# Kernel optimization log

Measured on AMD Instinct MI355X. Metric: run time of the kernel, lower is better.

## Reference

```python
import jax, jax.numpy as jnp
import numpy as np

GAMMA = 1.4
EX = jnp.array([1.0, 0.0], dtype=jnp.float32)
EY = jnp.array([0.0, 1.0], dtype=jnp.float32)


def _mlp(x, Ws, bs):
    h = x
    for W, b in zip(Ws[:-1], bs[:-1]):
        h = jnp.tanh(h @ W + b)
    return h @ Ws[-1] + bs[-1]


def setup_inputs() -> dict:
    key = jax.random.key(0)
    ks = jax.random.split(key, 24)
    N, NB = 32768, 4096
    inp = {}
    dom = jnp.array([1.5, 1.0], dtype=jnp.float32)
    inp['x_train'] = jax.random.uniform(ks[0], (N, 2), dtype=jnp.float32) * dom
    inp['x_inlet'] = jax.random.uniform(ks[1], (NB, 2), dtype=jnp.float32) * dom
    inp['U_inlet'] = jax.random.normal(ks[2], (NB, 4), dtype=jnp.float32)
    inp['x_base'] = jax.random.uniform(ks[3], (NB, 2), dtype=jnp.float32) * dom
    inp['x_top'] = jax.random.uniform(ks[4], (NB, 2), dtype=jnp.float32) * dom
    inp['x_slipNormal'] = jax.random.uniform(ks[5], (NB, 2), dtype=jnp.float32) * dom
    dims = [2, 128, 128, 128, 128, 4]
    for i in range(5):
        fan_in = dims[i]
        inp[f'W{i}'] = jax.random.normal(ks[6 + i], (dims[i], dims[i + 1]), dtype=jnp.float32) / jnp.sqrt(jnp.float32(fan_in))
        inp[f'b{i}'] = jnp.zeros((dims[i + 1],), dtype=jnp.float32)
    d2 = [2, 64, 64, 1]
    for i in range(3):
        inp[f'V{i}'] = jax.random.normal(ks[12 + i], (d2[i], d2[i + 1]), dtype=jnp.float32) / jnp.sqrt(jnp.float32(d2[i]))
        inp[f'c{i}'] = jnp.zeros((d2[i + 1],), dtype=jnp.float32)
    return inp


def reference(x_train, x_inlet, U_inlet, x_base, x_top, x_slipNormal,
              W0, b0, W1, b1, W2, b2, W3, b3, W4, b4,
              V0, c0, V1, c1, V2, c2):
    Ws = [W0, W1, W2, W3, W4]
    bs = [b0, b1, b2, b3, b4]
    Vs = [V0, V1, V2]
    cs = [c0, c1, c2]

    def fields(xy):
        # per-point: returns [U1..U4, f1..f4, g1..g4] (12,)
        rho, p, u, v = _mlp(xy, Ws, bs)
        E = p / (GAMMA - 1.0) + 0.5 * rho * (u * u + v * v)
        return jnp.stack([
            rho, rho * u, rho * v, E,                               # U
            rho * u, rho * u * u + p, rho * u * v, u * (E + p),     # f (x-flux)
            rho * v, rho * u * v, rho * v * v + p, v * (E + p)])    # g (y-flux)

    def dUx(xy):
        return jax.jvp(fields, (xy,), (EX,))[1][:4]

    def dUy(xy):
        return jax.jvp(fields, (xy,), (EY,))[1][:4]

    def point_residual(xy):
        _, dx = jax.jvp(fields, (xy,), (EX,))   # x-derivs of all 12 fields
        _, dy = jax.jvp(fields, (xy,), (EY,))   # y-derivs
        U_xx = jax.jvp(dUx, (xy,), (EX,))[1]    # second derivs (fwd-over-fwd)
        U_yy = jax.jvp(dUy, (xy,), (EY,))[1]
        mu = 0.01 * _mlp(xy, Vs, cs)[0] ** 2
        res = dx[4:8] + dy[8:12] - mu * (U_xx + U_yy)  # (4,)
        return res, mu

    res, mu = jax.vmap(point_residual)(x_train)  # res: (N,4), mu: (N,)
    physics = jnp.sum(jnp.mean(res ** 2, axis=0))  # r1+r2+r3+r4

    out_in = _mlp(x_inlet, Ws, bs)
    inlet = jnp.sum(jnp.mean((out_in - U_inlet) ** 2, axis=0))

    base = jnp.mean(_mlp(x_base, Ws, bs)[:, 3] ** 2)
    top = jnp.mean(_mlp(x_top, Ws, bs)[:, 3] ** 2)

    ang = -jnp.pi / 18.0
    o = _mlp(x_slipNormal, Ws, bs)
    slip = jnp.mean((-o[:, 2] * jnp.sin(ang) + o[:, 3] * jnp.cos(ang)) ** 2)

    total = physics + 10.0 * (inlet + base + top + slip) + 0.1 * jnp.mean(mu ** 2)
    return total
```

## Files before the change

### kernel.cpp

```cpp
#include <hip/hip_runtime.h>

#define NTRAIN 32768
#define NBDY   4096
#define PHYS_BLOCKS (NTRAIN / 64)
#define BDY_BLOCKS  128

#define LDS_BYTES 71680

typedef _Float16 f16x8 __attribute__((ext_vector_type(8)));
typedef __fp16   fp16x2 __attribute__((ext_vector_type(2)));
typedef float    f32x4 __attribute__((ext_vector_type(4)));

union FragU { uint4 q; f16x8 b; _Float16 e[8]; };
union F4  { float4 v; float f[4]; };
union H2  { fp16x2 h; _Float16 e[2]; unsigned int u; };

__device__ __forceinline__ float fast_tanh(float z) {
    float e = __expf(2.0f * z);
    return 1.0f - 2.0f * __builtin_amdgcn_rcpf(e + 1.0f);
}

__device__ __forceinline__ unsigned int pk2(float a, float b) {
    H2 r; r.h = __builtin_amdgcn_cvt_pkrtz(a, b);
    return r.u;
}

__global__ __launch_bounds__(256) void pack_w_kernel(
    const float* __restrict__ W1, const float* __restrict__ W2,
    const float* __restrict__ W3, const float* __restrict__ V1,
    const float* __restrict__ W4,
    unsigned short* __restrict__ wsU, float* __restrict__ out)
{
    int b = blockIdx.x;
    if (b < 24) {
        int mat = b >> 3, rb = b & 7;
        const float* W = (mat == 0) ? W1 : (mat == 1) ? W2 : W3;
        unsigned int* hiU = (unsigned int*)(wsU + mat * 32768);
        unsigned int* loU = hiU + 8192;
        int n   = threadIdx.x & 127;
        int pr0 = threadIdx.x >> 7;
        #pragma unroll
        for (int it = 0; it < 4; it++) {
            int pr = pr0 + 2 * it;
            int k  = rb * 16 + pr * 2;
            float v0 = W[k * 128 + n];
            float v1 = W[(k + 1) * 128 + n];
            H2 hh, ll;
            hh.e[0] = (_Float16)v0;
            hh.e[1] = (_Float16)v1;
            ll.e[0] = (_Float16)(v0 - (float)hh.e[0]);
            ll.e[1] = (_Float16)(v1 - (float)hh.e[1]);
            int base = ((n >> 4) * 4 + (k >> 5)) * 64 + ((k >> 3) & 3) * 16 + (n & 15);
            int uoff = base * 4 + ((k & 7) >> 1);
            hiU[uoff] = hh.u;
            loU[uoff] = ll.u;
        }
    } else if (b == 24) {
        unsigned int* hiU = (unsigned int*)(wsU + 98304);
        int n   = threadIdx.x & 63;
        int pr0 = threadIdx.x >> 6;
        #pragma unroll
        for (int it = 0; it < 8; it++) {
            int pr = pr0 + 4 * it;
            int k  = pr * 2;
            float v0 = V1[k * 64 + n];
            float v1 = V1[(k + 1) * 64 + n];
            H2 hh;
            hh.e[0] = (_Float16)v0;
            hh.e[1] = (_Float16)v1;
            int base = ((n >> 4) * 2 + (k >> 5)) * 64 + ((k >> 3) & 3) * 16 + (n & 15);
            hiU[base * 4 + ((k & 7) >> 1)] = hh.u;
        }
        if (threadIdx.x == 0) out[0] = 0.f;
    } else {
        _Float16* hi = (_Float16*)(wsU + 102400);
        _Float16* lo = hi + 2048;
        int u4 = threadIdx.x;
        int lane = u4 & 63, ks = u4 >> 6;
        int m  = lane & 15;
        int kb = ks * 32 + ((lane >> 4) << 3);
        FragU fh, fl;
        #pragma unroll
        for (int j = 0; j < 8; j++) {
            float v = (m < 4) ? W4[(kb + j) * 4 + m] : 0.f;
            _Float16 h = (_Float16)v;
            fh.e[j] = h;
            fl.e[j] = (_Float16)(v - (float)h);
        }
        *(uint4*)(hi + u4 * 8) = fh.q;
        *(uint4*)(lo + u4 * 8) = fl.q;
    }
}

__global__ __launch_bounds__(512, 4) void fused_kernel(
    const float* __restrict__ xt,
    const float* __restrict__ x_inlet, const float* __restrict__ U_inlet,
    const float* __restrict__ x_base,  const float* __restrict__ x_top,
    const float* __restrict__ x_slip,
    const float* __restrict__ W0, const float* __restrict__ b0,
    const float* __restrict__ W1, const float* __restrict__ b1,
    const float* __restrict__ W2, const float* __restrict__ b2,
    const float* __restrict__ W3, const float* __restrict__ b3,
    const float* __restrict__ W4, const float* __restrict__ b4,
    const float* __restrict__ V0, const float* __restrict__ c0,
    const float* __restrict__ V1, const float* __restrict__ c1,
    const float* __restrict__ V2, const float* __restrict__ c2,
    const unsigned short* __restrict__ wsU,
    float* __restrict__ out)
{
    extern __shared__ char SMC[];
    unsigned short* AhU = (unsigned short*)SMC;
    float* MUPART = (float*)(SMC + 69632);
    float* BIASF  = (float*)(SMC + 70144);

    const int t = threadIdx.x;
    const int wv   = t >> 6;
    const int lane = t & 63;
    const int nn   = lane & 15;
    const int q    = lane >> 4;

    if (blockIdx.x < PHYS_BLOCKS) {
        const int blk = blockIdx.x;

        if (t < 128) {
            BIASF[t]       = b1[t];
            BIASF[128 + t] = b2[t];
            BIASF[256 + t] = b3[t];
        }

        {
            const int g = wv >> 1, h = wv & 1;
            const float2 xyn = *(const float2*)(xt + (blk * 64 + g * 16 + nn) * 2);
            FragU mb[2];
            #pragma unroll
            for (int ks = 0; ks < 2; ks++) {
                int u0 = ks * 32 + q * 8;
                F4 va0, va1, vb0, vb1, cc0, cc1;
                va0.v = *(const float4*)(V0 + u0);
                va1.v = *(const float4*)(V0 + u0 + 4);
                vb0.v = *(const float4*)(V0 + 64 + u0);
                vb1.v = *(const float4*)(V0 + 64 + u0 + 4);
                cc0.v = *(const float4*)(c0 + u0);
                cc1.v = *(const float4*)(c0 + u0 + 4);
                #pragma unroll
                for (int i = 0; i < 4; i++) {
                    mb[ks].e[i]     = (_Float16)fast_tanh(
                        xyn.x * va0.f[i] + xyn.y * vb0.f[i] + cc0.f[i]);
                    mb[ks].e[4 + i] = (_Float16)fast_tanh(
                        xyn.x * va1.f[i] + xyn.y * vb1.f[i] + cc1.f[i]);
                }
            }
            float partial = 0.f;
            #pragma unroll
            for (int i = 0; i < 2; i++) {
                f32x4 macc = {0.f, 0.f, 0.f, 0.f};
                #pragma unroll
                for (int ks = 0; ks < 2; ks++) {
                    FragU vh;
                    vh.q = *(const uint4*)(wsU + 98304 +
                           ((((2 * h + i) * 2 + ks) * 64 + lane) << 3));
                    macc = __builtin_amdgcn_mfma_f32_16x16x32_f16(vh.b, mb[ks].b, macc, 0, 0, 0);
                }
                int u2 = (2 * h + i) * 16 + q * 4;
                F4 cv, w2;
                cv.v = *(const float4*)(c1 + u2);
                w2.v = *(const float4*)(V2 + u2);
                #pragma unroll
                for (int r = 0; r < 4; r++)
                    partial += fast_tanh(macc[r] + cv.f[r]) * w2.f[r];
            }
            partial += __shfl_xor(partial, 16);
            partial += __shfl_xor(partial, 32);
            if (lane < 16) MUPART[wv * 16 + nn] = partial;
        }
        {
            const int pl = t >> 4, c = t & 15;
            #pragma unroll
            for (int h2 = 0; h2 < 2; h2++) {
                const int p = h2 * 32 + pl;
                const float2 xy = *(const float2*)(xt + (blk * 64 + p) * 2);
                const float x = xy.x, y = xy.y;
                float vals[4][8];
                #pragma unroll
                for (int j = 0; j < 8; j++) {
                    int u = c * 8 + j;
                    float w0 = W0[u], w1 = W0[128 + u];
                    float zv = x * w0 + y * w1 + b0[u];
                    float tt = fast_tanh(zv);
                    float s2 = 1.f - tt * tt;
                    float m2 = -2.f * tt * s2;
                    vals[0][j] = tt;
                    vals[1][j] = s2 * w0;
                    vals[2][j] = s2 * w1;
                    vals[3][j] = m2 * (w0 * w0 + w1 * w1);
                }
                const int g = p >> 4, p15 = p & 15;
                #pragma unroll
                for (int s = 0; s < 4; s++) {
                    uint4 d = make_uint4(pk2(vals[s][0], vals[s][1]),
                                         pk2(vals[s][2], vals[s][3]),
                                         pk2(vals[s][4], vals[s][5]),
                                         pk2(vals[s][6], vals[s][7]));
                    *(uint4*)(AhU + ((g * 4 + s) * 16 + p15) * 136 + c * 8) = d;
                }
            }
        }
        __syncthreads();

        #pragma unroll 1
        for (int l = 0; l < 3; l++) {
            const unsigned short* WpL = wsU + l * 32768;
            f32x4 acc[16];
            #pragma unroll
            for (int s = 0; s < 16; s++) {
                acc[s][0] = 0.f; acc[s][1] = 0.f;
                acc[s][2] = 0.f; acc[s][3] = 0.f;
            }
            FragU wh[4];
            #pragma unroll
            for (int ks = 0; ks < 4; ks++)
                wh[ks].q = *(const uint4*)(WpL + (((wv * 4 + ks) * 64 + lane) << 3));
            #pragma unroll
            for (int ks = 0; ks < 4; ks++) {
                #pragma unroll
                for (int s = 0; s < 16; s++) {
                    FragU bh;
                    bh.q = *(const uint4*)(AhU + (s * 16 + nn) * 136 + ks * 32 + q * 8);
                    acc[s] = __builtin_amdgcn_mfma_f32_16x16x32_f16(
                        wh[ks].b, bh.b, acc[s], 0, 0, 0);
                }
            }
            __syncthreads();
            const int ubase = wv * 16 + q * 4;
            F4 bv; bv.v = *(const float4*)&BIASF[l * 128 + ubase];
            #pragma unroll
            for (int g = 0; g < 4; g++) {
                float vals[4][4];
                #pragma unroll
                for (int r = 0; r < 4; r++) {
                    float z  = acc[g * 4 + 0][r] + bv.f[r];
                    float zx = acc[g * 4 + 1][r];
                    float zy = acc[g * 4 + 2][r];
                    float zl = acc[g * 4 + 3][r];
                    float tt = fast_tanh(z);
                    float s2 = 1.f - tt * tt;
                    float m2 = -2.f * tt * s2;
                    vals[0][r] = tt;
                    vals[1][r] = s2 * zx;
                    vals[2][r] = s2 * zy;
                    vals[3][r] = s2 * zl + m2 * (zx * zx + zy * zy);
                }
                #pragma unroll
                for (int s = 0; s < 4; s++) {
                    uint2 d = make_uint2(pk2(vals[s][0], vals[s][1]),
                                         pk2(vals[s][2], vals[s][3]));
                    *(uint2*)(AhU + ((g * 4 + s) * 16 + nn) * 136 + ubase) = d;
                }
            }
            __syncthreads();
        }

        {
            const unsigned short* W4p = wsU + 102400;
            const int rtA = wv, rtB = 8 + wv;
            f32x4 aA = {0.f, 0.f, 0.f, 0.f};
            f32x4 aB = {0.f, 0.f, 0.f, 0.f};
            #pragma unroll
            for (int ks = 0; ks < 4; ks++) {
                FragU wh, wl, bA, bB;
                const unsigned short* base = W4p + ((ks * 64 + lane) << 3);
                wh.q = *(const uint4*)base;
                wl.q = *(const uint4*)(base + 2048);
                bA.q = *(const uint4*)(AhU + (rtA * 16 + nn) * 136 + ks * 32 + q * 8);
                bB.q = *(const uint4*)(AhU + (rtB * 16 + nn) * 136 + ks * 32 + q * 8);
                aA = __builtin_amdgcn_mfma_f32_16x16x32_f16(wh.b, bA.b, aA, 0, 0, 0);
                aA = __builtin_amdgcn_mfma_f32_16x16x32_f16(wl.b, bA.b, aA, 0, 0, 0);
                aB = __builtin_amdgcn_mfma_f32_16x16x32_f16(wh.b, bB.b, aB, 0, 0, 0);
                aB = __builtin_amdgcn_mfma_f32_16x16x32_f16(wl.b, bB.b, aB, 0, 0, 0);
            }
            if (q == 0) {
                float4 oA = make_float4(aA[0], aA[1], aA[2], aA[3]);
                float4 oB = make_float4(aB[0], aB[1], aB[2], aB[3]);
                if ((rtA & 3) == 0) {
                    oA.x += b4[0]; oA.y += b4[1]; oA.z += b4[2]; oA.w += b4[3];
                }
                if ((rtB & 3) == 0) {
                    oB.x += b4[0]; oB.y += b4[1]; oB.z += b4[2]; oB.w += b4[3];
                }
                *(float4*)(SMC + (rtA * 16 + nn) * 272 + 256) = oA;
                *(float4*)(SMC + (rtB * 16 + nn) * 272 + 256) = oB;
            }
        }
        __syncthreads();

        float contrib = 0.f;
        if (t < 64) {
            const int pp = t, g = pp >> 4, p15 = pp & 15;
            F4 V, DX, DY, LAP;
            V.v   = *(const float4*)(SMC + ((g * 4 + 0) * 16 + p15) * 272 + 256);
            DX.v  = *(const float4*)(SMC + ((g * 4 + 1) * 16 + p15) * 272 + 256);
            DY.v  = *(const float4*)(SMC + ((g * 4 + 2) * 16 + p15) * 272 + 256);
            LAP.v = *(const float4*)(SMC + ((g * 4 + 3) * 16 + p15) * 272 + 256);
            float r = V.f[0],  P = V.f[1],  u = V.f[2],  v = V.f[3];
            float rx = DX.f[0], Px = DX.f[1], ux = DX.f[2], vx = DX.f[3];
            float ry = DY.f[0], Py = DY.f[1], uy = DY.f[2], vy = DY.f[3];
            float rl = LAP.f[0], Pl = LAP.f[1], ul = LAP.f[2], vl = LAP.f[3];
            const float GI = 2.5f;

            float s = MUPART[(2 * g) * 16 + p15] + MUPART[(2 * g + 1) * 16 + p15]
                    + c2[0];
            float mu = 0.01f * s * s;

            float q2 = u * u + v * v;
            float E  = P * GI + 0.5f * r * q2;
            float Ex = Px * GI + 0.5f * rx * q2 + r * (u * ux + v * vx);
            float Ey = Py * GI + 0.5f * ry * q2 + r * (u * uy + v * vy);
            float EpP = E + P;

            float f1x = rx * u + r * ux;
            float f2x = rx * u * u + 2.f * r * u * ux + Px;
            float f3x = rx * u * v + r * ux * v + r * u * vx;
            float f4x = ux * EpP + u * (Ex + Px);

            float g1y = ry * v + r * vy;
            float g2y = ry * u * v + r * uy * v + r * u * vy;
            float g3y = ry * v * v + 2.f * r * v * vy + Py;
            float g4y = vy * EpP + v * (Ey + Py);

            float qx  = 2.f * (u * ux + v * vx);
            float qy  = 2.f * (u * uy + v * vy);
            float ql  = 2.f * (ux * ux + uy * uy + vx * vx + vy * vy)
                      + 2.f * (u * ul + v * vl);

            float U1s = rl;
            float U2s = rl * u + 2.f * (rx * ux + ry * uy) + r * ul;
            float U3s = rl * v + 2.f * (rx * vx + ry * vy) + r * vl;
            float U4s = Pl * GI
                      + 0.5f * (rl * q2 + 2.f * (rx * qx + ry * qy) + r * ql);

            float r1 = f1x + g1y - mu * U1s;
            float r2 = f2x + g2y - mu * U2s;
            float r3 = f3x + g3y - mu * U3s;
            float r4 = f4x + g4y - mu * U4s;

            contrib = (r1 * r1 + r2 * r2 + r3 * r3 + r4 * r4 + 0.1f * mu * mu)
                      * (1.0f / (float)NTRAIN);
        }
        if (t < 64) {
            contrib += __shfl_down(contrib, 32);
            contrib += __shfl_down(contrib, 16);
            contrib += __shfl_down(contrib, 8);
            contrib += __shfl_down(contrib, 4);
            contrib += __shfl_down(contrib, 2);
            contrib += __shfl_down(contrib, 1);
            if (t == 0) atomicAdd(out, contrib);
        }
    } else {
        const int bb    = blockIdx.x - PHYS_BLOCKS;
        const int batch = bb >> 5;
        const int lb    = bb & 31;
        const float* xs = (batch == 0) ? x_inlet
                        : (batch == 1) ? x_base
                        : (batch == 2) ? x_top : x_slip;
        const int base_pt = lb * 128;

        {
            int p2 = t & 127, ug = t >> 7;
            float2 xy = *(const float2*)(xs + (base_pt + p2) * 2);
            float x = xy.x, y = xy.y;
            #pragma unroll
            for (int g = 0; g < 8; g++) {
                int u0 = ug * 32 + g * 4;
                F4 wa, wb, bbv;
                wa.v  = *(const float4*)(W0 + u0);
                wb.v  = *(const float4*)(W0 + 128 + u0);
                bbv.v = *(const float4*)(b0 + u0);
                float t0 = fast_tanh(x * wa.f[0] + y * wb.f[0] + bbv.f[0]);
                float t1 = fast_tanh(x * wa.f[1] + y * wb.f[1] + bbv.f[1]);
                float t2 = fast_tanh(x * wa.f[2] + y * wb.f[2] + bbv.f[2]);
                float t3 = fast_tanh(x * wa.f[3] + y * wb.f[3] + bbv.f[3]);
                uint2 d = make_uint2(pk2(t0, t1), pk2(t2, t3));
                *(uint2*)(AhU + p2 * 136 + u0) = d;
            }
            if (t < 128) {
                BIASF[t]       = b1[t];
                BIASF[128 + t] = b2[t];
                BIASF[256 + t] = b3[t];
            }
        }
        __syncthreads();

        #pragma unroll 1
        for (int l = 0; l < 3; l++) {
            const unsigned short* WpL = wsU + l * 32768;
            f32x4 acc[8];
            #pragma unroll
            for (int n = 0; n < 8; n++) {
                acc[n][0] = 0.f; acc[n][1] = 0.f;
                acc[n][2] = 0.f; acc[n][3] = 0.f;
            }
            FragU wh[4];
            #pragma unroll
            for (int ks = 0; ks < 4; ks++)
                wh[ks].q = *(const uint4*)(WpL + (((wv * 4 + ks) * 64 + lane) << 3));
            #pragma unroll
            for (int ks = 0; ks < 4; ks++) {
                #pragma unroll
                for (int n = 0; n < 8; n++) {
                    FragU bh;
                    bh.q = *(const uint4*)(AhU + (n * 16 + nn) * 136 + ks * 32 + q * 8);
                    acc[n] = __builtin_amdgcn_mfma_f32_16x16x32_f16(
                        wh[ks].b, bh.b, acc[n], 0, 0, 0);
                }
            }
            __syncthreads();
            const int ubase = wv * 16 + q * 4;
            F4 bv; bv.v = *(const float4*)&BIASF[l * 128 + ubase];
            #pragma unroll
            for (int n = 0; n < 8; n++) {
                float t0 = fast_tanh(acc[n][0] + bv.f[0]);
                float t1 = fast_tanh(acc[n][1] + bv.f[1]);
                float t2 = fast_tanh(acc[n][2] + bv.f[2]);
                float t3 = fast_tanh(acc[n][3] + bv.f[3]);
                uint2 d = make_uint2(pk2(t0, t1), pk2(t2, t3));
                *(uint2*)(AhU + (n * 16 + nn) * 136 + ubase) = d;
            }
            __syncthreads();
        }

        {
            const unsigned short* W4p = wsU + 102400;
            f32x4 a4 = {0.f, 0.f, 0.f, 0.f};
            #pragma unroll
            for (int ks = 0; ks < 4; ks++) {
                FragU bh, wh, wl;
                bh.q = *(const uint4*)(AhU + (wv * 16 + nn) * 136 + ks * 32 + q * 8);
                const unsigned short* base = W4p + ((ks * 64 + lane) << 3);
                wh.q = *(const uint4*)base;
                wl.q = *(const uint4*)(base + 2048);
                a4 = __builtin_amdgcn_mfma_f32_16x16x32_f16(wh.b, bh.b, a4, 0, 0, 0);
                a4 = __builtin_amdgcn_mfma_f32_16x16x32_f16(wl.b, bh.b, a4, 0, 0, 0);
            }
            if (q == 0) {
                float4 o = make_float4(a4[0] + b4[0], a4[1] + b4[1],
                                       a4[2] + b4[2], a4[3] + b4[3]);
                *(float4*)(SMC + (wv * 16 + nn) * 272 + 256) = o;
            }
        }
        __syncthreads();

        if (t < 128) {
            F4 O; O.v = *(const float4*)(SMC + t * 272 + 256);
            float o0 = O.f[0], o1 = O.f[1], o2 = O.f[2], o3 = O.f[3];
            float l;
            if (batch == 0) {
                float4 Ui = *(const float4*)(U_inlet + (base_pt + t) * 4);
                float d0 = o0 - Ui.x, d1 = o1 - Ui.y, d2 = o2 - Ui.z, d3 = o3 - Ui.w;
                l = d0 * d0 + d1 * d1 + d2 * d2 + d3 * d3;
            } else if (batch == 3) {
                const float sa = -0.17364817766693033f;
                const float ca =  0.9848077530122080f;
                float d = -o2 * sa + o3 * ca;
                l = d * d;
            } else {
                l = o3 * o3;
            }
            float contrib = 10.0f * l * (1.0f / (float)NBDY);
            contrib += __shfl_down(contrib, 32);
            contrib += __shfl_down(contrib, 16);
            contrib += __shfl_down(contrib, 8);
            contrib += __shfl_down(contrib, 4);
            contrib += __shfl_down(contrib, 2);
            contrib += __shfl_down(contrib, 1);
            if ((t & 63) == 0) atomicAdd(out, contrib);
        }
    }
}

extern "C" void kernel_launch(void* const* d_in, const int* in_sizes, int n_in,
                              void* d_out, int out_size, void* d_ws, size_t ws_size,
                              hipStream_t stream) {
    const float* xt      = (const float*)d_in[0];
    const float* x_inlet = (const float*)d_in[1];
    const float* U_inlet = (const float*)d_in[2];
    const float* x_base  = (const float*)d_in[3];
    const float* x_top   = (const float*)d_in[4];
    const float* x_slip  = (const float*)d_in[5];
    const float* W0 = (const float*)d_in[6];
    const float* b0 = (const float*)d_in[7];
    const float* W1 = (const float*)d_in[8];
    const float* b1 = (const float*)d_in[9];
    const float* W2 = (const float*)d_in[10];
    const float* b2 = (const float*)d_in[11];
    const float* W3 = (const float*)d_in[12];
    const float* b3 = (const float*)d_in[13];
    const float* W4 = (const float*)d_in[14];
    const float* b4 = (const float*)d_in[15];
    const float* V0 = (const float*)d_in[16];
    const float* c0 = (const float*)d_in[17];
    const float* V1 = (const float*)d_in[18];
    const float* c1 = (const float*)d_in[19];
    const float* V2 = (const float*)d_in[20];
    const float* c2 = (const float*)d_in[21];
    float* out = (float*)d_out;
    unsigned short* wsU = (unsigned short*)d_ws;

    pack_w_kernel<<<26, 256, 0, stream>>>(W1, W2, W3, V1, W4, wsU, out);

    (void)hipFuncSetAttribute((const void*)fused_kernel,
                              hipFuncAttributeMaxDynamicSharedMemorySize,
                              LDS_BYTES);
    fused_kernel<<<PHYS_BLOCKS + BDY_BLOCKS, 512, LDS_BYTES, stream>>>(
        xt, x_inlet, U_inlet, x_base, x_top, x_slip,
        W0, b0, W1, b1, W2, b2, W3, b3, W4, b4,
        V0, c0, V1, c1, V2, c2, wsU, out);
}
```

Baseline: 130.0 us.

## Tile hidden-layer MFMA work into 2D unit-by-point blocks per wave

Result: slower. 134.2 us (+3.2%).

```diff
diff --git a/kernel.cpp b/kernel.cpp
--- a/kernel.cpp
+++ b/kernel.cpp
@@ -210,38 +210,46 @@
         #pragma unroll 1
         for (int l = 0; l < 3; l++) {
             const unsigned short* WpL = wsU + l * 32768;
-            f32x4 acc[16];
-            #pragma unroll
-            for (int s = 0; s < 16; s++) {
-                acc[s][0] = 0.f; acc[s][1] = 0.f;
-                acc[s][2] = 0.f; acc[s][3] = 0.f;
-            }
-            FragU wh[4];
-            #pragma unroll
-            for (int ks = 0; ks < 4; ks++)
-                wh[ks].q = *(const uint4*)(WpL + (((wv * 4 + ks) * 64 + lane) << 3));
+            const int uh = wv & 1;
+            const int g  = wv >> 1;
+            f32x4 acc[4][4];
+            #pragma unroll
+            for (int u = 0; u < 4; u++)
+                #pragma unroll
+                for (int s = 0; s < 4; s++) {
+                    acc[u][s][0] = 0.f; acc[u][s][1] = 0.f;
+                    acc[u][s][2] = 0.f; acc[u][s][3] = 0.f;
+                }
             #pragma unroll
             for (int ks = 0; ks < 4; ks++) {
-                #pragma unroll
-                for (int s = 0; s < 16; s++) {
-                    FragU bh;
-                    bh.q = *(const uint4*)(AhU + (s * 16 + nn) * 136 + ks * 32 + q * 8);
-                    acc[s] = __builtin_amdgcn_mfma_f32_16x16x32_f16(
-                        wh[ks].b, bh.b, acc[s], 0, 0, 0);
-                }
+                FragU wh[4], bh[4];
+                #pragma unroll
+                for (int u = 0; u < 4; u++)
+                    wh[u].q = *(const uint4*)(WpL +
+                        (((((uh * 4 + u) * 4) + ks) * 64 + lane) << 3));
+                #pragma unroll
+                for (int s = 0; s < 4; s++)
+                    bh[s].q = *(const uint4*)(AhU +
+                        ((g * 4 + s) * 16 + nn) * 136 + ks * 32 + q * 8);
+                #pragma unroll
+                for (int u = 0; u < 4; u++)
+                    #pragma unroll
+                    for (int s = 0; s < 4; s++)
+                        acc[u][s] = __builtin_amdgcn_mfma_f32_16x16x32_f16(
+                            wh[u].b, bh[s].b, acc[u][s], 0, 0, 0);
             }
             __syncthreads();
-            const int ubase = wv * 16 + q * 4;
-            F4 bv; bv.v = *(const float4*)&BIASF[l * 128 + ubase];
-            #pragma unroll
-            for (int g = 0; g < 4; g++) {
+            #pragma unroll
+            for (int u = 0; u < 4; u++) {
+                const int ubase = (uh * 4 + u) * 16 + q * 4;
+                F4 bv; bv.v = *(const float4*)&BIASF[l * 128 + ubase];
                 float vals[4][4];
                 #pragma unroll
                 for (int r = 0; r < 4; r++) {
-                    float z  = acc[g * 4 + 0][r] + bv.f[r];
-                    float zx = acc[g * 4 + 1][r];
-                    float zy = acc[g * 4 + 2][r];
-                    float zl = acc[g * 4 + 3][r];
+                    float z  = acc[u][0][r] + bv.f[r];
+                    float zx = acc[u][1][r];
+                    float zy = acc[u][2][r];
+                    float zl = acc[u][3][r];
                     float tt = fast_tanh(z);
                     float s2 = 1.f - tt * tt;
                     float m2 = -2.f * tt * s2;
@@ -393,37 +401,48 @@
         #pragma unroll 1
         for (int l = 0; l < 3; l++) {
             const unsigned short* WpL = wsU + l * 32768;
-            f32x4 acc[8];
-            #pragma unroll
-            for (int n = 0; n < 8; n++) {
-                acc[n][0] = 0.f; acc[n][1] = 0.f;
-                acc[n][2] = 0.f; acc[n][3] = 0.f;
-            }
-            FragU wh[4];
-            #pragma unroll
-            for (int ks = 0; ks < 4; ks++)
-                wh[ks].q = *(const uint4*)(WpL + (((wv * 4 + ks) * 64 + lane) << 3));
+            const int up = wv & 3;
+            const int rh = wv >> 2;
+            f32x4 acc[2][4];
+            #pragma unroll
+            for (int u = 0; u < 2; u++)
+                #pragma unroll
+                for (int n = 0; n < 4; n++) {
+                    acc[u][n][0] = 0.f; acc[u][n][1] = 0.f;
+                    acc[u][n][2] = 0.f; acc[u][n][3] = 0.f;
+                }
             #pragma unroll
             for (int ks = 0; ks < 4; ks++) {
-                #pragma unroll
-                for (int n = 0; n < 8; n++) {
-                    FragU bh;
-                    bh.q = *(const uint4*)(AhU + (n * 16 + nn) * 136 + ks * 32 + q * 8);
-                    acc[n] = __builtin_amdgcn_mfma_f32_16x16x32_f16(
-                        wh[ks].b, bh.b, acc[n], 0, 0, 0);
-                }
+                FragU wh[2], bh[4];
+                #pragma unroll
+                for (int u = 0; u < 2; u++)
+                    wh[u].q = *(const uint4*)(WpL +
+                        (((((up * 2 + u) * 4) + ks) * 64 + lane) << 3));
+                #pragma unroll
+                for (int n = 0; n < 4; n++)
+                    bh[n].q = *(const uint4*)(AhU +
+                        ((rh * 4 + n) * 16 + nn) * 136 + ks * 32 + q * 8);
+                #pragma unroll
+                for (int u = 0; u < 2; u++)
+                    #pragma unroll
+                    for (int n = 0; n < 4; n++)
+                        acc[u][n] = __builtin_amdgcn_mfma_f32_16x16x32_f16(
+                            wh[u].b, bh[n].b, acc[u][n], 0, 0, 0);
             }
             __syncthreads();
-            const int ubase = wv * 16 + q * 4;
-            F4 bv; bv.v = *(const float4*)&BIASF[l * 128 + ubase];
-            #pragma unroll
-            for (int n = 0; n < 8; n++) {
-                float t0 = fast_tanh(acc[n][0] + bv.f[0]);
-                float t1 = fast_tanh(acc[n][1] + bv.f[1]);
-                float t2 = fast_tanh(acc[n][2] + bv.f[2]);
-                float t3 = fast_tanh(acc[n][3] + bv.f[3]);
-                uint2 d = make_uint2(pk2(t0, t1), pk2(t2, t3));
-                *(uint2*)(AhU + (n * 16 + nn) * 136 + ubase) = d;
+            #pragma unroll
+            for (int u = 0; u < 2; u++) {
+                const int ubase = (up * 2 + u) * 16 + q * 4;
+                F4 bv; bv.v = *(const float4*)&BIASF[l * 128 + ubase];
+                #pragma unroll
+                for (int n = 0; n < 4; n++) {
+                    float t0 = fast_tanh(acc[u][n][0] + bv.f[0]);
+                    float t1 = fast_tanh(acc[u][n][1] + bv.f[1]);
+                    float t2 = fast_tanh(acc[u][n][2] + bv.f[2]);
+                    float t3 = fast_tanh(acc[u][n][3] + bv.f[3]);
+                    uint2 d = make_uint2(pk2(t0, t1), pk2(t2, t3));
+                    *(uint2*)(AhU + ((rh * 4 + n) * 16 + nn) * 136 + ubase) = d;
+                }
             }
             __syncthreads();
         }
```

## Merge boundary points into uniform 256-thread blocks alongside 32 physics points each

Applied to the files above, without the earlier changes.

Measured after the change: 146.7 us. +12.9%, slower.

```diff
diff --git a/kernel.cpp b/kernel.cpp
--- a/kernel.cpp
+++ b/kernel.cpp
@@ -2,10 +2,7 @@
 
 #define NTRAIN 32768
 #define NBDY   4096
-#define PHYS_BLOCKS (NTRAIN / 64)
-#define BDY_BLOCKS  128
-
-#define LDS_BYTES 71680
+#define NBLK   1024
 
 typedef _Float16 f16x8 __attribute__((ext_vector_type(8)));
 typedef __fp16   fp16x2 __attribute__((ext_vector_type(2)));
@@ -92,7 +89,7 @@
     }
 }
 
-__global__ __launch_bounds__(512, 4) void fused_kernel(
+__global__ __launch_bounds__(256, 4) void fused_kernel(
     const float* __restrict__ xt,
     const float* __restrict__ x_inlet, const float* __restrict__ U_inlet,
     const float* __restrict__ x_base,  const float* __restrict__ x_top,
@@ -108,10 +105,10 @@
     const unsigned short* __restrict__ wsU,
     float* __restrict__ out)
 {
-    extern __shared__ char SMC[];
-    unsigned short* AhU = (unsigned short*)SMC;
-    float* MUPART = (float*)(SMC + 69632);
-    float* BIASF  = (float*)(SMC + 70144);
+    __shared__ float SM[9856];
+    unsigned short* AhU = (unsigned short*)SM;
+    float* MUPART = SM + 9792;
+    #define OUTF4(r) ((float4*)((char*)SM + (r) * 272 + 256))
 
     const int t = threadIdx.x;
     const int wv   = t >> 6;
@@ -119,129 +116,147 @@
     const int nn   = lane & 15;
     const int q    = lane >> 4;
 
-    if (blockIdx.x < PHYS_BLOCKS) {
-        const int blk = blockIdx.x;
-
-        if (t < 128) {
-            BIASF[t]       = b1[t];
-            BIASF[128 + t] = b2[t];
-            BIASF[256 + t] = b3[t];
-        }
-
-        {
-            const int g = wv >> 1, h = wv & 1;
-            const float2 xyn = *(const float2*)(xt + (blk * 64 + g * 16 + nn) * 2);
-            FragU mb[2];
+    const int blk   = blockIdx.x;
+    const int batch = blk >> 8;
+    const int bbase = (blk & 255) * 16;
+    const float* xs = (batch == 0) ? x_inlet
+                    : (batch == 1) ? x_base
+                    : (batch == 2) ? x_top : x_slip;
+
+    {
+        const int g = wv >> 1, h = wv & 1;
+        const float2 xyn = *(const float2*)(xt + (blk * 32 + g * 16 + nn) * 2);
+        FragU mb[2];
+        #pragma unroll
+        for (int ks = 0; ks < 2; ks++) {
+            int u0 = ks * 32 + q * 8;
+            F4 va0, va1, vb0, vb1, cc0, cc1;
+            va0.v = *(const float4*)(V0 + u0);
+            va1.v = *(const float4*)(V0 + u0 + 4);
+            vb0.v = *(const float4*)(V0 + 64 + u0);
+            vb1.v = *(const float4*)(V0 + 64 + u0 + 4);
+            cc0.v = *(const float4*)(c0 + u0);
+            cc1.v = *(const float4*)(c0 + u0 + 4);
+            #pragma unroll
+            for (int i = 0; i < 4; i++) {
+                mb[ks].e[i]     = (_Float16)fast_tanh(
+                    xyn.x * va0.f[i] + xyn.y * vb0.f[i] + cc0.f[i]);
+                mb[ks].e[4 + i] = (_Float16)fast_tanh(
+                    xyn.x * va1.f[i] + xyn.y * vb1.f[i] + cc1.f[i]);
+            }
+        }
+        float partial = 0.f;
+        #pragma unroll
+        for (int i = 0; i < 2; i++) {
+            f32x4 macc = {0.f, 0.f, 0.f, 0.f};
             #pragma unroll
             for (int ks = 0; ks < 2; ks++) {
-                int u0 = ks * 32 + q * 8;
-                F4 va0, va1, vb0, vb1, cc0, cc1;
-                va0.v = *(const float4*)(V0 + u0);
-                va1.v = *(const float4*)(V0 + u0 + 4);
-                vb0.v = *(const float4*)(V0 + 64 + u0);
-                vb1.v = *(const float4*)(V0 + 64 + u0 + 4);
-                cc0.v = *(const float4*)(c0 + u0);
-                cc1.v = *(const float4*)(c0 + u0 + 4);
-                #pragma unroll
-                for (int i = 0; i < 4; i++) {
-                    mb[ks].e[i]     = (_Float16)fast_tanh(
-                        xyn.x * va0.f[i] + xyn.y * vb0.f[i] + cc0.f[i]);
-                    mb[ks].e[4 + i] = (_Float16)fast_tanh(
-                        xyn.x * va1.f[i] + xyn.y * vb1.f[i] + cc1.f[i]);
-                }
-            }
-            float partial = 0.f;
-            #pragma unroll
-            for (int i = 0; i < 2; i++) {
-                f32x4 macc = {0.f, 0.f, 0.f, 0.f};
-                #pragma unroll
-                for (int ks = 0; ks < 2; ks++) {
-                    FragU vh;
-                    vh.q = *(const uint4*)(wsU + 98304 +
-                           ((((2 * h + i) * 2 + ks) * 64 + lane) << 3));
-                    macc = __builtin_amdgcn_mfma_f32_16x16x32_f16(vh.b, mb[ks].b, macc, 0, 0, 0);
-                }
-                int u2 = (2 * h + i) * 16 + q * 4;
-                F4 cv, w2;
-                cv.v = *(const float4*)(c1 + u2);
-                w2.v = *(const float4*)(V2 + u2);
-                #pragma unroll
-                for (int r = 0; r < 4; r++)
-                    partial += fast_tanh(macc[r] + cv.f[r]) * w2.f[r];
-            }
-            partial += __shfl_xor(partial, 16);
-            partial += __shfl_xor(partial, 32);
-            if (lane < 16) MUPART[wv * 16 + nn] = partial;
-        }
-        {
-            const int pl = t >> 4, c = t & 15;
-            #pragma unroll
-            for (int h2 = 0; h2 < 2; h2++) {
-                const int p = h2 * 32 + pl;
-                const float2 xy = *(const float2*)(xt + (blk * 64 + p) * 2);
-                const float x = xy.x, y = xy.y;
-                float vals[4][8];
-                #pragma unroll
-                for (int j = 0; j < 8; j++) {
-                    int u = c * 8 + j;
-                    float w0 = W0[u], w1 = W0[128 + u];
-                    float zv = x * w0 + y * w1 + b0[u];
-                    float tt = fast_tanh(zv);
-                    float s2 = 1.f - tt * tt;
-                    float m2 = -2.f * tt * s2;
-                    vals[0][j] = tt;
-                    vals[1][j] = s2 * w0;
-                    vals[2][j] = s2 * w1;
-                    vals[3][j] = m2 * (w0 * w0 + w1 * w1);
-                }
-                const int g = p >> 4, p15 = p & 15;
-                #pragma unroll
-                for (int s = 0; s < 4; s++) {
-                    uint4 d = make_uint4(pk2(vals[s][0], vals[s][1]),
-                                         pk2(vals[s][2], vals[s][3]),
-                                         pk2(vals[s][4], vals[s][5]),
-                                         pk2(vals[s][6], vals[s][7]));
-                    *(uint4*)(AhU + ((g * 4 + s) * 16 + p15) * 136 + c * 8) = d;
-                }
+                FragU vh;
+                vh.q = *(const uint4*)(wsU + 98304 +
+                       ((((2 * h + i) * 2 + ks) * 64 + lane) << 3));
+                macc = __builtin_amdgcn_mfma_f32_16x16x32_f16(vh.b, mb[ks].b, macc, 0, 0, 0);
+            }
+            int u2 = (2 * h + i) * 16 + q * 4;
+            F4 cv, w2;
+            cv.v = *(const float4*)(c1 + u2);
+            w2.v = *(const float4*)(V2 + u2);
+            #pragma unroll
+            for (int r = 0; r < 4; r++)
+                partial += fast_tanh(macc[r] + cv.f[r]) * w2.f[r];
+        }
+        partial += __shfl_xor(partial, 16);
+        partial += __shfl_xor(partial, 32);
+        if (lane < 16) MUPART[wv * 16 + nn] = partial;
+    }
+
+    {
+        const int pl = t >> 4, c = t & 15;
+        #pragma unroll
+        for (int h2 = 0; h2 < 2; h2++) {
+            const int p = h2 * 16 + pl;
+            const float2 xy = *(const float2*)(xt + (blk * 32 + p) * 2);
+            const float x = xy.x, y = xy.y;
+            float vals[4][8];
+            #pragma unroll
+            for (int j = 0; j < 8; j++) {
+                int u = c * 8 + j;
+                float w0 = W0[u], w1 = W0[128 + u];
+                float zv = x * w0 + y * w1 + b0[u];
+                float tt = fast_tanh(zv);
+                float s2 = 1.f - tt * tt;
+                float m2 = -2.f * tt * s2;
+                vals[0][j] = tt;
+                vals[1][j] = s2 * w0;
+                vals[2][j] = s2 * w1;
+                vals[3][j] = m2 * (w0 * w0 + w1 * w1);
+            }
+            #pragma unroll
+            for (int s = 0; s < 4; s++) {
+                uint4 d = make_uint4(pk2(vals[s][0], vals[s][1]),
+                                     pk2(vals[s][2], vals[s][3]),
+                                     pk2(vals[s][4], vals[s][5]),
+                                     pk2(vals[s][6], vals[s][7]));
+                *(uint4*)(AhU + ((h2 * 4 + s) * 16 + pl) * 136 + c * 8) = d;
+            }
+        }
+    }
+    {
+        const int pl = t >> 4, c = t & 15;
+        const float2 xy = *(const float2*)(xs + (bbase + pl) * 2);
+        float tv[8];
+        #pragma unroll
+        for (int j = 0; j < 8; j++) {
+            int u = c * 8 + j;
+            tv[j] = fast_tanh(xy.x * W0[u] + xy.y * W0[128 + u] + b0[u]);
+        }
+        uint4 d = make_uint4(pk2(tv[0], tv[1]), pk2(tv[2], tv[3]),
+                             pk2(tv[4], tv[5]), pk2(tv[6], tv[7]));
+        *(uint4*)(AhU + (128 + pl) * 136 + c * 8) = d;
+    }
+    __syncthreads();
+
+    #pragma unroll 1
+    for (int l = 0; l < 3; l++) {
+        const unsigned short* WpL = wsU + l * 32768;
+        const float* bl = (l == 0) ? b1 : (l == 1) ? b2 : b3;
+        f32x4 acc[2][9];
+        #pragma unroll
+        for (int i = 0; i < 2; i++)
+            #pragma unroll
+            for (int s = 0; s < 9; s++) {
+                acc[i][s][0] = 0.f; acc[i][s][1] = 0.f;
+                acc[i][s][2] = 0.f; acc[i][s][3] = 0.f;
+            }
+        #pragma unroll
+        for (int ks = 0; ks < 4; ks++) {
+            FragU wh[2];
+            #pragma unroll
+            for (int i = 0; i < 2; i++)
+                wh[i].q = *(const uint4*)(WpL + ((((2 * wv + i) * 4 + ks) * 64 + lane) << 3));
+            #pragma unroll
+            for (int s = 0; s < 9; s++) {
+                FragU bh;
+                bh.q = *(const uint4*)(AhU + (s * 16 + nn) * 136 + ks * 32 + q * 8);
+                acc[0][s] = __builtin_amdgcn_mfma_f32_16x16x32_f16(
+                    wh[0].b, bh.b, acc[0][s], 0, 0, 0);
+                acc[1][s] = __builtin_amdgcn_mfma_f32_16x16x32_f16(
+                    wh[1].b, bh.b, acc[1][s], 0, 0, 0);
             }
         }
         __syncthreads();
-
-        #pragma unroll 1
-        for (int l = 0; l < 3; l++) {
-            const unsigned short* WpL = wsU + l * 32768;
-            f32x4 acc[16];
-            #pragma unroll
-            for (int s = 0; s < 16; s++) {
-                acc[s][0] = 0.f; acc[s][1] = 0.f;
-                acc[s][2] = 0.f; acc[s][3] = 0.f;
-            }
-            FragU wh[4];
-            #pragma unroll
-            for (int ks = 0; ks < 4; ks++)
-                wh[ks].q = *(const uint4*)(WpL + (((wv * 4 + ks) * 64 + lane) << 3));
-            #pragma unroll
-            for (int ks = 0; ks < 4; ks++) {
-                #pragma unroll
-                for (int s = 0; s < 16; s++) {
-                    FragU bh;
-                    bh.q = *(const uint4*)(AhU + (s * 16 + nn) * 136 + ks * 32 + q * 8);
-                    acc[s] = __builtin_amdgcn_mfma_f32_16x16x32_f16(
-                        wh[ks].b, bh.b, acc[s], 0, 0, 0);
-                }
-            }
-            __syncthreads();
-            const int ubase = wv * 16 + q * 4;
-            F4 bv; bv.v = *(const float4*)&BIASF[l * 128 + ubase];
-            #pragma unroll
-            for (int g = 0; g < 4; g++) {
+        #pragma unroll
+        for (int i = 0; i < 2; i++) {
+            const int ubase = (2 * wv + i) * 16 + q * 4;
+            F4 bv; bv.v = *(const float4*)(bl + ubase);
+            #pragma unroll
+            for (int g = 0; g < 2; g++) {
                 float vals[4][4];
                 #pragma unroll
                 for (int r = 0; r < 4; r++) {
-                    float z  = acc[g * 4 + 0][r] + bv.f[r];
-                    float zx = acc[g * 4 + 1][r];
-                    float zy = acc[g * 4 + 2][r];
-                    float zl = acc[g * 4 + 3][r];
+                    float z  = acc[i][g * 4 + 0][r] + bv.f[r];
+                    float zx = acc[i][g * 4 + 1][r];
+                    float zy = acc[i][g * 4 + 2][r];
+                    float zl = acc[i][g * 4 + 3][r];
                     float tt = fast_tanh(z);
                     float s2 = 1.f - tt * tt;
                     float m2 = -2.f * tt * s2;
@@ -257,224 +272,142 @@
                     *(uint2*)(AhU + ((g * 4 + s) * 16 + nn) * 136 + ubase) = d;
                 }
             }
-            __syncthreads();
-        }
-
-        {
-            const unsigned short* W4p = wsU + 102400;
-            const int rtA = wv, rtB = 8 + wv;
-            f32x4 aA = {0.f, 0.f, 0.f, 0.f};
-            f32x4 aB = {0.f, 0.f, 0.f, 0.f};
-            #pragma unroll
-            for (int ks = 0; ks < 4; ks++) {
-                FragU wh, wl, bA, bB;
-                const unsigned short* base = W4p + ((ks * 64 + lane) << 3);
-                wh.q = *(const uint4*)base;
-                wl.q = *(const uint4*)(base + 2048);
-                bA.q = *(const uint4*)(AhU + (rtA * 16 + nn) * 136 + ks * 32 + q * 8);
-                bB.q = *(const uint4*)(AhU + (rtB * 16 + nn) * 136 + ks * 32 + q * 8);
-                aA = __builtin_amdgcn_mfma_f32_16x16x32_f16(wh.b, bA.b, aA, 0, 0, 0);
-                aA = __builtin_amdgcn_mfma_f32_16x16x32_f16(wl.b, bA.b, aA, 0, 0, 0);
-                aB = __builtin_amdgcn_mfma_f32_16x16x32_f16(wh.b, bB.b, aB, 0, 0, 0);
-                aB = __builtin_amdgcn_mfma_f32_16x16x32_f16(wl.b, bB.b, aB, 0, 0, 0);
-            }
-            if (q == 0) {
-                float4 oA = make_float4(aA[0], aA[1], aA[2], aA[3]);
-                float4 oB = make_float4(aB[0], aB[1], aB[2], aB[3]);
-                if ((rtA & 3) == 0) {
-                    oA.x += b4[0]; oA.y += b4[1]; oA.z += b4[2]; oA.w += b4[3];
-                }
-                if ((rtB & 3) == 0) {
-                    oB.x += b4[0]; oB.y += b4[1]; oB.z += b4[2]; oB.w += b4[3];
-                }
-                *(float4*)(SMC + (rtA * 16 + nn) * 272 + 256) = oA;
-                *(float4*)(SMC + (rtB * 16 + nn) * 272 + 256) = oB;
+            {
+                float t0 = fast_tanh(acc[i][8][0] + bv.f[0]);
+                float t1 = fast_tanh(acc[i][8][1] + bv.f[1]);
+                float t2 = fast_tanh(acc[i][8][2] + bv.f[2]);
+                float t3 = fast_tanh(acc[i][8][3] + bv.f[3]);
+                uint2 d = make_uint2(pk2(t0, t1), pk2(t2, t3));
+                *(uint2*)(AhU + (128 + nn) * 136 + ubase) = d;
             }
         }
         __syncthreads();
-
-        float contrib = 0.f;
-        if (t < 64) {
-            const int pp = t, g = pp >> 4, p15 = pp & 15;
-            F4 V, DX, DY, LAP;
-            V.v   = *(const float4*)(SMC + ((g * 4 + 0) * 16 + p15) * 272 + 256);
-            DX.v  = *(const float4*)(SMC + ((g * 4 + 1) * 16 + p15) * 272 + 256);
-            DY.v  = *(const float4*)(SMC + ((g * 4 + 2) * 16 + p15) * 272 + 256);
-            LAP.v = *(const float4*)(SMC + ((g * 4 + 3) * 16 + p15) * 272 + 256);
-            float r = V.f[0],  P = V.f[1],  u = V.f[2],  v = V.f[3];
-            float rx = DX.f[0], Px = DX.f[1], ux = DX.f[2], vx = DX.f[3];
-            float ry = DY.f[0], Py = DY.f[1], uy = DY.f[2], vy = DY.f[3];
-            float rl = LAP.f[0], Pl = LAP.f[1], ul = LAP.f[2], vl = LAP.f[3];
-            const float GI = 2.5f;
-
-            float s = MUPART[(2 * g) * 16 + p15] + MUPART[(2 * g + 1) * 16 + p15]
-                    + c2[0];
-            float mu = 0.01f * s * s;
-
-            float q2 = u * u + v * v;
-            float E  = P * GI + 0.5f * r * q2;
-            float Ex = Px * GI + 0.5f * rx * q2 + r * (u * ux + v * vx);
-            float Ey = Py * GI + 0.5f * ry * q2 + r * (u * uy + v * vy);
-            float EpP = E + P;
-
-            float f1x = rx * u + r * ux;
-            float f2x = rx * u * u + 2.f * r * u * ux + Px;
-            float f3x = rx * u * v + r * ux * v + r * u * vx;
-            float f4x = ux * EpP + u * (Ex + Px);
-
-            float g1y = ry * v + r * vy;
-            float g2y = ry * u * v + r * uy * v + r * u * vy;
-            float g3y = ry * v * v + 2.f * r * v * vy + Py;
-            float g4y = vy * EpP + v * (Ey + Py);
-
-            float qx  = 2.f * (u * ux + v * vx);
-            float qy  = 2.f * (u * uy + v * vy);
-            float ql  = 2.f * (ux * ux + uy * uy + vx * vx + vy * vy)
-                      + 2.f * (u * ul + v * vl);
-
-            float U1s = rl;
-            float U2s = rl * u + 2.f * (rx * ux + ry * uy) + r * ul;
-            float U3s = rl * v + 2.f * (rx * vx + ry * vy) + r * vl;
-            float U4s = Pl * GI
-                      + 0.5f * (rl * q2 + 2.f * (rx * qx + ry * qy) + r * ql);
-
-            float r1 = f1x + g1y - mu * U1s;
-            float r2 = f2x + g2y - mu * U2s;
-            float r3 = f3x + g3y - mu * U3s;
-            float r4 = f4x + g4y - mu * U4s;
-
-            contrib = (r1 * r1 + r2 * r2 + r3 * r3 + r4 * r4 + 0.1f * mu * mu)
-                      * (1.0f / (float)NTRAIN);
-        }
-        if (t < 64) {
-            contrib += __shfl_down(contrib, 32);
-            contrib += __shfl_down(contrib, 16);
-            contrib += __shfl_down(contrib, 8);
-            contrib += __shfl_down(contrib, 4);
-            contrib += __shfl_down(contrib, 2);
-            contrib += __shfl_down(contrib, 1);
-            if (t == 0) atomicAdd(out, contrib);
-        }
-    } else {
-        const int bb    = blockIdx.x - PHYS_BLOCKS;
-        const int batch = bb >> 5;
-        const int lb    = bb & 31;
-        const float* xs = (batch == 0) ? x_inlet
-                        : (batch == 1) ? x_base
-                        : (batch == 2) ? x_top : x_slip;
-        const int base_pt = lb * 128;
-
-        {
-            int p2 = t & 127, ug = t >> 7;
-            float2 xy = *(const float2*)(xs + (base_pt + p2) * 2);
-            float x = xy.x, y = xy.y;
-            #pragma unroll
-            for (int g = 0; g < 8; g++) {
-                int u0 = ug * 32 + g * 4;
-                F4 wa, wb, bbv;
-                wa.v  = *(const float4*)(W0 + u0);
-                wb.v  = *(const float4*)(W0 + 128 + u0);
-                bbv.v = *(const float4*)(b0 + u0);
-                float t0 = fast_tanh(x * wa.f[0] + y * wb.f[0] + bbv.f[0]);
-                float t1 = fast_tanh(x * wa.f[1] + y * wb.f[1] + bbv.f[1]);
-                float t2 = fast_tanh(x * wa.f[2] + y * wb.f[2] + bbv.f[2]);
-                float t3 = fast_tanh(x * wa.f[3] + y * wb.f[3] + bbv.f[3]);
-                uint2 d = make_uint2(pk2(t0, t1), pk2(t2, t3));
-                *(uint2*)(AhU + p2 * 136 + u0) = d;
-            }
-            if (t < 128) {
-                BIASF[t]       = b1[t];
-                BIASF[128 + t] = b2[t];
-                BIASF[256 + t] = b3[t];
-            }
-        }
-        __syncthreads();
-
-        #pragma unroll 1
-        for (int l = 0; l < 3; l++) {
-            const unsigned short* WpL = wsU + l * 32768;
-            f32x4 acc[8];
-            #pragma unroll
-            for (int n = 0; n < 8; n++) {
-                acc[n][0] = 0.f; acc[n][1] = 0.f;
-                acc[n][2] = 0.f; acc[n][3] = 0.f;
-            }
-            FragU wh[4];
-            #pragma unroll
-            for (int ks = 0; ks < 4; ks++)
-                wh[ks].q = *(const uint4*)(WpL + (((wv * 4 + ks) * 64 + lane) << 3));
-            #pragma unroll
-            for (int ks = 0; ks < 4; ks++) {
-                #pragma unroll
-                for (int n = 0; n < 8; n++) {
-                    FragU bh;
-                    bh.q = *(const uint4*)(AhU + (n * 16 + nn) * 136 + ks * 32 + q * 8);
-                    acc[n] = __builtin_amdgcn_mfma_f32_16x16x32_f16(
-                        wh[ks].b, bh.b, acc[n], 0, 0, 0);
-                }
-            }
-            __syncthreads();
-            const int ubase = wv * 16 + q * 4;
-            F4 bv; bv.v = *(const float4*)&BIASF[l * 128 + ubase];
-            #pragma unroll
-            for (int n = 0; n < 8; n++) {
-                float t0 = fast_tanh(acc[n][0] + bv.f[0]);
-                float t1 = fast_tanh(acc[n][1] + bv.f[1]);
-                float t2 = fast_tanh(acc[n][2] + bv.f[2]);
-                float t3 = fast_tanh(acc[n][3] + bv.f[3]);
-                uint2 d = make_uint2(pk2(t0, t1), pk2(t2, t3));
-                *(uint2*)(AhU + (n * 16 + nn) * 136 + ubase) = d;
-            }
-            __syncthreads();
-        }
-
-        {
-            const unsigned short* W4p = wsU + 102400;
-            f32x4 a4 = {0.f, 0.f, 0.f, 0.f};
-            #pragma unroll
-            for (int ks = 0; ks < 4; ks++) {
-                FragU bh, wh, wl;
-                bh.q = *(const uint4*)(AhU + (wv * 16 + nn) * 136 + ks * 32 + q * 8);
-                const unsigned short* base = W4p + ((ks * 64 + lane) << 3);
-                wh.q = *(const uint4*)base;
-                wl.q = *(const uint4*)(base + 2048);
-                a4 = __builtin_amdgcn_mfma_f32_16x16x32_f16(wh.b, bh.b, a4, 0, 0, 0);
-                a4 = __builtin_amdgcn_mfma_f32_16x16x32_f16(wl.b, bh.b, a4, 0, 0, 0);
-            }
-            if (q == 0) {
-                float4 o = make_float4(a4[0] + b4[0], a4[1] + b4[1],
-                                       a4[2] + b4[2], a4[3] + b4[3]);
-                *(float4*)(SMC + (wv * 16 + nn) * 272 + 256) = o;
-            }
-        }
-        __syncthreads();
-
-        if (t < 128) {
-            F4 O; O.v = *(const float4*)(SMC + t * 272 + 256);
-            float o0 = O.f[0], o1 = O.f[1], o2 = O.f[2], o3 = O.f[3];
-            float l;
-            if (batch == 0) {
-                float4 Ui = *(const float4*)(U_inlet + (base_pt + t) * 4);
-                float d0 = o0 - Ui.x, d1 = o1 - Ui.y, d2 = o2 - Ui.z, d3 = o3 - Ui.w;
-                l = d0 * d0 + d1 * d1 + d2 * d2 + d3 * d3;
-            } else if (batch == 3) {
-                const float sa = -0.17364817766693033f;
-                const float ca =  0.9848077530122080f;
-                float d = -o2 * sa + o3 * ca;
-                l = d * d;
-            } else {
-                l = o3 * o3;
-            }
-            float contrib = 10.0f * l * (1.0f / (float)NBDY);
-            contrib += __shfl_down(contrib, 32);
-            contrib += __shfl_down(contrib, 16);
-            contrib += __shfl_down(contrib, 8);
-            contrib += __shfl_down(contrib, 4);
-            contrib += __shfl_down(contrib, 2);
-            contrib += __shfl_down(contrib, 1);
-            if ((t & 63) == 0) atomicAdd(out, contrib);
-        }
-    }
+    }
+
+    {
+        const unsigned short* W4p = wsU + 102400;
+        const int rtA = wv, rtB = 4 + wv;
+        f32x4 aA = {0.f, 0.f, 0.f, 0.f};
+        f32x4 aB = {0.f, 0.f, 0.f, 0.f};
+        f32x4 aC = {0.f, 0.f, 0.f, 0.f};
+        #pragma unroll
+        for (int ks = 0; ks < 4; ks++) {
+            FragU wh, wl, bA, bB;
+            const unsigned short* base = W4p + ((ks * 64 + lane) << 3);
+            wh.q = *(const uint4*)base;
+            wl.q = *(const uint4*)(base + 2048);
+            bA.q = *(const uint4*)(AhU + (rtA * 16 + nn) * 136 + ks * 32 + q * 8);
+            bB.q = *(const uint4*)(AhU + (rtB * 16 + nn) * 136 + ks * 32 + q * 8);
+            aA = __builtin_amdgcn_mfma_f32_16x16x32_f16(wh.b, bA.b, aA, 0, 0, 0);
+            aA = __builtin_amdgcn_mfma_f32_16x16x32_f16(wl.b, bA.b, aA, 0, 0, 0);
+            aB = __builtin_amdgcn_mfma_f32_16x16x32_f16(wh.b, bB.b, aB, 0, 0, 0);
+            aB = __builtin_amdgcn_mfma_f32_16x16x32_f16(wl.b, bB.b, aB, 0, 0, 0);
+            if (wv == 3) {
+                FragU bC;
+                bC.q = *(const uint4*)(AhU + (128 + nn) * 136 + ks * 32 + q * 8);
+                aC = __builtin_amdgcn_mfma_f32_16x16x32_f16(wh.b, bC.b, aC, 0, 0, 0);
+                aC = __builtin_amdgcn_mfma_f32_16x16x32_f16(wl.b, bC.b, aC, 0, 0, 0);
+            }
+        }
+        if (q == 0) {
+            float4 oA = make_float4(aA[0], aA[1], aA[2], aA[3]);
+            float4 oB = make_float4(aB[0], aB[1], aB[2], aB[3]);
+            if (wv == 0) {
+                oA.x += b4[0]; oA.y += b4[1]; oA.z += b4[2]; oA.w += b4[3];
+                oB.x += b4[0]; oB.y += b4[1]; oB.z += b4[2]; oB.w += b4[3];
+            }
+            *OUTF4(rtA * 16 + nn) = oA;
+            *OUTF4(rtB * 16 + nn) = oB;
+            if (wv == 3) {
+                float4 oC = make_float4(aC[0] + b4[0], aC[1] + b4[1],
+                                        aC[2] + b4[2], aC[3] + b4[3]);
+                *OUTF4(128 + nn) = oC;
+            }
+        }
+    }
+    __syncthreads();
+
+    float contrib = 0.f;
+    if (t < 32) {
+        const int pp = t, g = pp >> 4, p15 = pp & 15;
+        F4 V, DX, DY, LAP;
+        V.v   = *OUTF4((g * 4 + 0) * 16 + p15);
+        DX.v  = *OUTF4((g * 4 + 1) * 16 + p15);
+        DY.v  = *OUTF4((g * 4 + 2) * 16 + p15);
+        LAP.v = *OUTF4((g * 4 + 3) * 16 + p15);
+        float r = V.f[0],  P = V.f[1],  u = V.f[2],  v = V.f[3];
+        float rx = DX.f[0], Px = DX.f[1], ux = DX.f[2], vx = DX.f[3];
+        float ry = DY.f[0], Py = DY.f[1], uy = DY.f[2], vy = DY.f[3];
+        float rl = LAP.f[0], Pl = LAP.f[1], ul = LAP.f[2], vl = LAP.f[3];
+        const float GI = 2.5f;
+
+        float s = MUPART[(2 * g) * 16 + p15] + MUPART[(2 * g + 1) * 16 + p15]
+                + c2[0];
+        float mu = 0.01f * s * s;
+
+        float q2 = u * u + v * v;
+        float E  = P * GI + 0.5f * r * q2;
+        float Ex = Px * GI + 0.5f * rx * q2 + r * (u * ux + v * vx);
+        float Ey = Py * GI + 0.5f * ry * q2 + r * (u * uy + v * vy);
+        float EpP = E + P;
+
+        float f1x = rx * u + r * ux;
+        float f2x = rx * u * u + 2.f * r * u * ux + Px;
+        float f3x = rx * u * v + r * ux * v + r * u * vx;
+        float f4x = ux * EpP + u * (Ex + Px);
+
+        float g1y = ry * v + r * vy;
+        float g2y = ry * u * v + r * uy * v + r * u * vy;
+        float g3y = ry * v * v + 2.f * r * v * vy + Py;
+        float g4y = vy * EpP + v * (Ey + Py);
+
+        float qx  = 2.f * (u * ux + v * vx);
+        float qy  = 2.f * (u * uy + v * vy);
+        float ql  = 2.f * (ux * ux + uy * uy + vx * vx + vy * vy)
+                  + 2.f * (u * ul + v * vl);
+
+        float U1s = rl;
+        float U2s = rl * u + 2.f * (rx * ux + ry * uy) + r * ul;
+        float U3s = rl * v + 2.f * (rx * vx + ry * vy) + r * vl;
+        float U4s = Pl * GI
+                  + 0.5f * (rl * q2 + 2.f * (rx * qx + ry * qy) + r * ql);
+
+        float r1 = f1x + g1y - mu * U1s;
+        float r2 = f2x + g2y - mu * U2s;
+        float r3 = f3x + g3y - mu * U3s;
+        float r4 = f4x + g4y - mu * U4s;
+
+        contrib = (r1 * r1 + r2 * r2 + r3 * r3 + r4 * r4 + 0.1f * mu * mu)
+                  * (1.0f / (float)NTRAIN);
+    } else if (t >= 192 && t < 208) {
+        const int pb = t - 192;
+        F4 O; O.v = *OUTF4(128 + pb);
+        float o0 = O.f[0], o1 = O.f[1], o2 = O.f[2], o3 = O.f[3];
+        float lv;
+        if (batch == 0) {
+            float4 Ui = *(const float4*)(U_inlet + (bbase + pb) * 4);
+            float d0 = o0 - Ui.x, d1 = o1 - Ui.y, d2 = o2 - Ui.z, d3 = o3 - Ui.w;
+            lv = d0 * d0 + d1 * d1 + d2 * d2 + d3 * d3;
+        } else if (batch == 3) {
+            const float sa = -0.17364817766693033f;
+            const float ca =  0.9848077530122080f;
+            float d = -o2 * sa + o3 * ca;
+            lv = d * d;
+        } else {
+            lv = o3 * o3;
+        }
+        contrib = 10.0f * lv * (1.0f / (float)NBDY);
+    }
+    if (wv == 0 || wv == 3) {
+        contrib += __shfl_down(contrib, 32);
+        contrib += __shfl_down(contrib, 16);
+        contrib += __shfl_down(contrib, 8);
+        contrib += __shfl_down(contrib, 4);
+        contrib += __shfl_down(contrib, 2);
+        contrib += __shfl_down(contrib, 1);
+        if (lane == 0) atomicAdd(out, contrib);
+    }
+    #undef OUTF4
 }
 
 extern "C" void kernel_launch(void* const* d_in, const int* in_sizes, int n_in,
@@ -507,10 +440,7 @@
 
     pack_w_kernel<<<26, 256, 0, stream>>>(W1, W2, W3, V1, W4, wsU, out);
 
-    (void)hipFuncSetAttribute((const void*)fused_kernel,
-                              hipFuncAttributeMaxDynamicSharedMemorySize,
-                              LDS_BYTES);
-    fused_kernel<<<PHYS_BLOCKS + BDY_BLOCKS, 512, LDS_BYTES, stream>>>(
+    fused_kernel<<<NBLK, 256, 0, stream>>>(
         xt, x_inlet, U_inlet, x_base, x_top, x_slip,
         W0, b0, W1, b1, W2, b2, W3, b3, W4, b4,
         V0, c0, V1, c1, V2, c2, wsU, out);
```
